# Kernel tuning notes

Hardware: AMD Instinct MI355X
Metric: run time of the kernel (lower is better)

Reference implementation:

```python
import jax, jax.numpy as jnp
import numpy as np

NUM_HEADS = 16
NUM_KV_GROUPS = 4
EPS = 1e-6


def _rms_norm(x, w):
    # normalize over last dim (head_dim)
    return x * jax.lax.rsqrt(jnp.mean(x * x, axis=-1, keepdims=True) + EPS) * w


def _rope_cos_sin(T, head_dim):
    half = head_dim // 2
    inv_freq = 1.0 / (10000.0 ** (jnp.arange(half, dtype=jnp.float32) / half))
    freqs = jnp.arange(T, dtype=jnp.float32)[:, None] * inv_freq[None, :]  # [T, half]
    cos = jnp.repeat(jnp.cos(freqs), 2, axis=-1)  # [T, head_dim]
    sin = jnp.repeat(jnp.sin(freqs), 2, axis=-1)
    return cos, sin


def _apply_rope(x, cos, sin):
    # x: [B, H, T, head_dim]; cos/sin broadcast over B,H
    x1 = x[..., ::2]
    x2 = x[..., 1::2]
    x_rot = jnp.stack([-x2, x1], axis=-1).reshape(x.shape)  # interleave (-x2, x1)
    return x * cos + x_rot * sin


def setup_inputs() -> dict:
    key = jax.random.key(0)
    ks = jax.random.split(key, 5)
    scale = lambda k, sh: jax.random.normal(k, sh, dtype=jnp.float32) * 0.02
    return {
        "x": jax.random.normal(ks[0], (4, 2048, 1024), dtype=jnp.float32),
        "Wq": scale(ks[1], (1024, 1024)),
        "Wk": scale(ks[2], (256, 1024)),
        "Wv": scale(ks[3], (256, 1024)),
        "Wo": scale(ks[4], (1024, 1024)),
        "qn_w": jnp.ones((64,), jnp.float32),
        "kn_w": jnp.ones((64,), jnp.float32),
    }


def reference(x, Wq, Wk, Wv, Wo, qn_w, kn_w):
    B, T, D = x.shape
    H, G = NUM_HEADS, NUM_KV_GROUPS
    hd = D // H

    # projections (torch Linear: y = x @ W.T), reshape to [B, heads, T, hd]
    q = (x @ Wq.T).reshape(B, T, H, hd).transpose(0, 2, 1, 3)
    k = (x @ Wk.T).reshape(B, T, G, hd).transpose(0, 2, 1, 3)
    v = (x @ Wv.T).reshape(B, T, G, hd).transpose(0, 2, 1, 3)

    # optional qk RMSNorm (qk_norm=True)
    q = _rms_norm(q, qn_w)
    k = _rms_norm(k, kn_w)

    # RoPE (position_offset = 0)
    cos, sin = _rope_cos_sin(T, hd)
    q = _apply_rope(q, cos, sin)
    k = _apply_rope(k, cos, sin)

    # GQA: expand kv heads to match query heads
    rep = H // G
    k = jnp.repeat(k, rep, axis=1)
    v = jnp.repeat(v, rep, axis=1)

    # causal SDPA
    scores = jnp.einsum('bhqd,bhkd->bhqk', q, k) / jnp.sqrt(jnp.float32(hd))
    causal = jnp.tril(jnp.ones((T, T), dtype=bool))
    scores = jnp.where(causal, scores, jnp.float32(-1e30))
    attn = jax.nn.softmax(scores, axis=-1)
    out = jnp.einsum('bhqk,bhkd->bhqd', attn, v)

    out = out.transpose(0, 2, 1, 3).reshape(B, T, D)
    return out @ Wo.T
```

## Files before the change

### kernel.cpp

```cpp
#include <hip/hip_runtime.h>

typedef unsigned short u16;
typedef __attribute__((ext_vector_type(8))) short bf16x8;
typedef __attribute__((ext_vector_type(4))) short bf16x4;
typedef __attribute__((ext_vector_type(4))) float f32x4;

#define GP(p) ((const __attribute__((address_space(1))) void*)(unsigned long long)(p))
#define LP(p) ((__attribute__((address_space(3))) void*)(unsigned int)(unsigned long long)(p))

#define QSCALE 0.180336879486998f
#define M_BIAS (-12.0f)

__device__ __forceinline__ u16 f2bf(float f) {
  union { float f; unsigned u; } v; v.f = f;
  unsigned r = v.u + 0x7fffu + ((v.u >> 16) & 1u);
  return (u16)(r >> 16);
}
__device__ __forceinline__ short f2bf_cvt(float f) {
  __bf16 b = (__bf16)f;
  return *reinterpret_cast<short*>(&b);
}

#if __has_builtin(__builtin_amdgcn_mfma_f32_16x16x16bf16_1k)
#define MFMA16(A, B, C) __builtin_amdgcn_mfma_f32_16x16x16bf16_1k((A), (B), (C), 0, 0, 0)
#elif __has_builtin(__builtin_amdgcn_mfma_f32_16x16x16_bf16)
#define MFMA16(A, B, C) __builtin_amdgcn_mfma_f32_16x16x16_bf16((A), (B), (C), 0, 0, 0)
#else
static __device__ __forceinline__ f32x4 mfma16_asm(bf16x4 a, bf16x4 b, f32x4 c) {
  asm volatile("v_mfma_f32_16x16x16_bf16 %0, %1, %2, %0" : "+v"(c) : "v"(a), "v"(b));
  return c;
}
#define MFMA16(A, B, C) mfma16_asm((A), (B), (C))
#endif

__global__ void cast_kernel(const float* __restrict__ in, u16* __restrict__ out, int n4) {
  int i = blockIdx.x * blockDim.x + threadIdx.x;
  int stride = gridDim.x * blockDim.x;
  for (; i < n4; i += stride) {
    float4 v = reinterpret_cast<const float4*>(in)[i];
    ushort4 o = make_ushort4(f2bf(v.x), f2bf(v.y), f2bf(v.z), f2bf(v.w));
    reinterpret_cast<ushort4*>(out)[i] = o;
  }
}

__global__ void cast_w_kernel(const float* __restrict__ Wq, const float* __restrict__ Wk,
                              const float* __restrict__ Wv, const float* __restrict__ Wo,
                              u16* __restrict__ Wcat, u16* __restrict__ Wob) {
  int i = blockIdx.x * 256 + threadIdx.x;
  const float* src; u16* dst; int off;
  if (i < 262144)      { src = Wq; dst = Wcat;           off = i; }
  else if (i < 327680) { src = Wk; dst = Wcat + 1048576; off = i - 262144; }
  else if (i < 393216) { src = Wv; dst = Wcat + 1310720; off = i - 327680; }
  else                 { src = Wo; dst = Wob;            off = i - 393216; }
  float4 v = reinterpret_cast<const float4*>(src)[off];
  reinterpret_cast<ushort4*>(dst)[off] =
      make_ushort4(f2bf(v.x), f2bf(v.y), f2bf(v.z), f2bf(v.w));
}

__global__ void rope_table_kernel(float* __restrict__ ctab, float* __restrict__ stab) {
  int i = blockIdx.x * 256 + threadIdx.x;
  int t = i >> 5, f = i & 31;
  float inv = exp2f((float)f * (-13.287712379549449f / 32.0f));
  float ang = (float)t * inv;
  float sv, cv;
  sincosf(ang, &sv, &cv);
  ctab[i] = cv;
  stab[i] = sv;
}

__launch_bounds__(256)
__global__ void gemm_qkv_kernel(const u16* __restrict__ A, const u16* __restrict__ W,
                                u16* __restrict__ qh, u16* __restrict__ kh,
                                u16* __restrict__ vh,
                                const float* __restrict__ qn_w, const float* __restrict__ kn_w,
                                const float* __restrict__ ctab, const float* __restrict__ stab) {
  __shared__ __align__(16) u16 As[128 * 64];
  __shared__ __align__(16) u16 Bs[128 * 64];
  const int tid = threadIdx.x;
  const int w = tid >> 6, l = tid & 63;
  const int lr = l & 15, lk = l >> 4;
  const int wr = w >> 1, wc = w & 1;
  const int m0 = blockIdx.x * 128, n0 = blockIdx.y * 128;
  f32x4 acc[4][4] = {};
  for (int k0 = 0; k0 < 1024; k0 += 64) {
#pragma unroll
    for (int i = 0; i < 4; ++i) {
      int c = i * 256 + tid;
      const u16* ga = A + (size_t)(m0 + (c >> 3)) * 1024 + k0 + (c & 7) * 8;
      __builtin_amdgcn_global_load_lds(GP(ga), LP((char*)As + (i * 256 + (tid & ~63)) * 16), 16, 0, 0);
      const u16* gb = W + (size_t)(n0 + (c >> 3)) * 1024 + k0 + (c & 7) * 8;
      __builtin_amdgcn_global_load_lds(GP(gb), LP((char*)Bs + (i * 256 + (tid & ~63)) * 16), 16, 0, 0);
    }
    asm volatile("s_waitcnt vmcnt(0)" ::: "memory");
    __syncthreads();
#pragma unroll
    for (int kk = 0; kk < 2; ++kk) {
      bf16x8 af[4], bfr[4];
#pragma unroll
      for (int fi = 0; fi < 4; ++fi)
        af[fi] = *reinterpret_cast<const bf16x8*>(&As[(wr * 64 + fi * 16 + lr) * 64 + kk * 32 + lk * 8]);
#pragma unroll
      for (int fj = 0; fj < 4; ++fj)
        bfr[fj] = *reinterpret_cast<const bf16x8*>(&Bs[(wc * 64 + fj * 16 + lr) * 64 + kk * 32 + lk * 8]);
#pragma unroll
      for (int fi = 0; fi < 4; ++fi)
#pragma unroll
        for (int fj = 0; fj < 4; ++fj)
          acc[fi][fj] = __builtin_amdgcn_mfma_f32_16x16x32_bf16(af[fi], bfr[fj], acc[fi][fj], 0, 0, 0);
    }
    __syncthreads();
  }
  const int ncol0 = n0 + wc * 64;
  if (ncol0 < 1280) {
    const bool isq = ncol0 < 1024;
    const float* wn = isq ? qn_w : kn_w;
    const float sc = isq ? QSCALE : 1.0f;
    float wv[4];
#pragma unroll
    for (int fj = 0; fj < 4; ++fj) wv[fj] = wn[fj * 16 + lr];
#pragma unroll
    for (int fi = 0; fi < 4; ++fi)
#pragma unroll
      for (int r = 0; r < 4; ++r) {
        float ss = 0.f;
#pragma unroll
        for (int fj = 0; fj < 4; ++fj) ss += acc[fi][fj][r] * acc[fi][fj][r];
        ss += __shfl_xor(ss, 1); ss += __shfl_xor(ss, 2);
        ss += __shfl_xor(ss, 4); ss += __shfl_xor(ss, 8);
        float rinv = rsqrtf(ss * (1.0f / 64.0f) + 1e-6f);
        int m = m0 + wr * 64 + fi * 16 + lk * 4 + r;
        int t = m & 2047, b = m >> 11;
#pragma unroll
        for (int fj = 0; fj < 4; ++fj) {
          float xn = acc[fi][fj][r] * rinv * wv[fj];
          float pr = __shfl_xor(xn, 1);
          float rot = (lr & 1) ? pr : -pr;
          int ci = t * 32 + fj * 8 + (lr >> 1);
          u16 outv = f2bf((xn * ctab[ci] + rot * stab[ci]) * sc);
          int n = ncol0 + fj * 16 + lr;
          if (isq) {
            int h = n >> 6, d = n & 63;
            qh[((size_t)((b * 16 + h) * 2048 + t)) * 64 + d] = outv;
          } else {
            int n2 = n - 1024, g = n2 >> 6, d = n2 & 63;
            kh[((size_t)((b * 4 + g) * 2048 + t)) * 64 + d] = outv;
          }
        }
      }
  } else {
#pragma unroll
    for (int fi = 0; fi < 4; ++fi)
#pragma unroll
      for (int fj = 0; fj < 4; ++fj)
#pragma unroll
        for (int r = 0; r < 4; ++r) {
          int m = m0 + wr * 64 + fi * 16 + lk * 4 + r;
          int n2 = ncol0 + fj * 16 + lr - 1280;
          int b = m >> 11, t = m & 2047;
          int g = n2 >> 6, d = n2 & 63;
          vh[((size_t)((b * 4 + g) * 2048 + t)) * 64 + d] = f2bf(acc[fi][fj][r]);
        }
  }
}

__launch_bounds__(256)
__global__ void vtrans_kernel(const u16* __restrict__ vh, u16* __restrict__ vt) {
  const int bg = blockIdx.y, t0 = blockIdx.x * 64;
  const u16* src = vh + ((size_t)bg * 2048 + t0) * 64;
  u16* dst = vt + (size_t)bg * 64 * 2048 + t0;
#pragma unroll
  for (int i = 0; i < 2; ++i) {
    int c = i * 256 + threadIdx.x;
    int d = c >> 3, kc = (c & 7) * 8;
    bf16x8 o;
#pragma unroll
    for (int j = 0; j < 8; ++j) o[j] = (short)src[(size_t)(kc + j) * 64 + d];
    *reinterpret_cast<bf16x8*>(&dst[(size_t)d * 2048 + kc]) = o;
  }
}

__launch_bounds__(256)
__global__ void attn_kernel(const u16* __restrict__ qh, const u16* __restrict__ kh,
                            const u16* __restrict__ vt, u16* __restrict__ ao) {
  __shared__ __align__(16) u16 Ks[2][64 * 64];
  __shared__ __align__(16) u16 Vts[2][64 * 64];
  const int tid = threadIdx.x, w = tid >> 6, l = tid & 63;
  const int lr = l & 15, lk = l >> 4;
  const int p = blockIdx.x, bh = blockIdx.y;
  const int b = bh >> 4, h = bh & 15, g = h >> 2;
  const u16* Qh = qh + ((size_t)((b * 16 + h) * 2048)) * 64;
  const u16* Kb = kh + ((size_t)((b * 4 + g) * 2048)) * 64;
  const u16* Vtb = vt + ((size_t)((b * 4 + g) * 64)) * 2048;
  const int swz = (lr & 7) * 8;

  auto stage = [&](int k0, int buf) {
#pragma unroll
    for (int i = 0; i < 2; ++i) {
      int c = i * 256 + tid;
      int row = c >> 3, scol = ((c & 7) ^ (row & 7)) * 8;
      const u16* gk = Kb + (size_t)(k0 + row) * 64 + scol;
      __builtin_amdgcn_global_load_lds(GP(gk), LP((char*)&Ks[buf][0] + (i * 256 + (tid & ~63)) * 16), 16, 0, 0);
      const u16* gv = Vtb + (size_t)row * 2048 + k0 + scol;
      __builtin_amdgcn_global_load_lds(GP(gv), LP((char*)&Vts[buf][0] + (i * 256 + (tid & ~63)) * 16), 16, 0, 0);
    }
  };

  int cur = 0;
  auto run_qtile = [&](int qt) {
    const int q0 = qt * 64;
    const u16* Qb = Qh + ((size_t)(q0 + w * 16)) * 64;
    const bf16x8 qf0 = *reinterpret_cast<const bf16x8*>(&Qb[lr * 64 + lk * 8]);
    const bf16x8 qf1 = *reinterpret_cast<const bf16x8*>(&Qb[lr * 64 + 32 + lk * 8]);
    f32x4 oacc[4] = {};
    float lrow = 0.f;
    stage(0, cur);
    asm volatile("s_waitcnt vmcnt(0)" ::: "memory");
    __builtin_amdgcn_s_barrier();
    for (int it = 0; it <= qt; ++it) {
      if (it < qt) stage((it + 1) * 64, cur ^ 1);
      f32x4 sacc[4];
#pragma unroll
      for (int fi = 0; fi < 4; ++fi)
#pragma unroll
        for (int r = 0; r < 4; ++r) sacc[fi][r] = M_BIAS;
      __builtin_amdgcn_s_setprio(1);
#pragma unroll
      for (int kk = 0; kk < 2; ++kk) {
        bf16x8 qf = kk ? qf1 : qf0;
#pragma unroll
        for (int fi = 0; fi < 4; ++fi) {
          bf16x8 kf = *reinterpret_cast<const bf16x8*>(
              &Ks[cur][(fi * 16 + lr) * 64 + ((kk * 32 + lk * 8) ^ swz)]);
          sacc[fi] = __builtin_amdgcn_mfma_f32_16x16x32_bf16(kf, qf, sacc[fi], 0, 0, 0);
        }
      }
      __builtin_amdgcn_s_setprio(0);
      if (it == qt) {
        int qloc = w * 16 + lr;
#pragma unroll
        for (int fi = 0; fi < 4; ++fi)
#pragma unroll
          for (int r = 0; r < 4; ++r)
            if (fi * 16 + lk * 4 + r > qloc) sacc[fi][r] = -1e30f;
      }
      float psum = 0.f;
      bf16x4 pb[4];
#pragma unroll
      for (int fi = 0; fi < 4; ++fi)
#pragma unroll
        for (int r = 0; r < 4; ++r) {
          float pv = exp2f(sacc[fi][r]);
          psum += pv;
          pb[fi][r] = f2bf_cvt(pv);
        }
      psum += __shfl_xor(psum, 16);
      psum += __shfl_xor(psum, 32);
      lrow += psum;
      __builtin_amdgcn_s_setprio(1);
#pragma unroll
      for (int fi = 0; fi < 4; ++fi)
#pragma unroll
        for (int db = 0; db < 4; ++db) {
          bf16x4 vf = *reinterpret_cast<const bf16x4*>(
              &Vts[cur][(db * 16 + lr) * 64 + ((fi * 16 + lk * 4) ^ swz)]);
          oacc[db] = MFMA16(vf, pb[fi], oacc[db]);
        }
      __builtin_amdgcn_s_setprio(0);
      asm volatile("s_waitcnt vmcnt(0)" ::: "memory");
      __builtin_amdgcn_s_barrier();
      cur ^= 1;
    }
    float inv = 1.0f / lrow;
#pragma unroll
    for (int db = 0; db < 4; ++db) {
      bf16x4 o;
#pragma unroll
      for (int r = 0; r < 4; ++r) o[r] = f2bf_cvt(oacc[db][r] * inv);
      *reinterpret_cast<bf16x4*>(
          &ao[((size_t)(b * 2048 + q0 + w * 16 + lr)) * 1024 + h * 64 + db * 16 + lk * 4]) = o;
    }
  };
  run_qtile(31 - p);
  run_qtile(p);
}

__launch_bounds__(256)
__global__ void gemm_out_kernel(const u16* __restrict__ A, const u16* __restrict__ W,
                                float* __restrict__ out) {
  __shared__ __align__(16) u16 As[128 * 64];
  __shared__ __align__(16) u16 Bs[128 * 64];
  const int tid = threadIdx.x;
  const int w = tid >> 6, l = tid & 63;
  const int lr = l & 15, lk = l >> 4;
  const int wr = w >> 1, wc = w & 1;
  const int m0 = blockIdx.x * 128, n0 = blockIdx.y * 128;
  f32x4 acc[4][4] = {};
  for (int k0 = 0; k0 < 1024; k0 += 64) {
#pragma unroll
    for (int i = 0; i < 4; ++i) {
      int c = i * 256 + tid;
      const u16* ga = A + (size_t)(m0 + (c >> 3)) * 1024 + k0 + (c & 7) * 8;
      __builtin_amdgcn_global_load_lds(GP(ga), LP((char*)As + (i * 256 + (tid & ~63)) * 16), 16, 0, 0);
      const u16* gb = W + (size_t)(n0 + (c >> 3)) * 1024 + k0 + (c & 7) * 8;
      __builtin_amdgcn_global_load_lds(GP(gb), LP((char*)Bs + (i * 256 + (tid & ~63)) * 16), 16, 0, 0);
    }
    asm volatile("s_waitcnt vmcnt(0)" ::: "memory");
    __syncthreads();
#pragma unroll
    for (int kk = 0; kk < 2; ++kk) {
      bf16x8 af[4], bfr[4];
#pragma unroll
      for (int fi = 0; fi < 4; ++fi)
        af[fi] = *reinterpret_cast<const bf16x8*>(&As[(wr * 64 + fi * 16 + lr) * 64 + kk * 32 + lk * 8]);
#pragma unroll
      for (int fj = 0; fj < 4; ++fj)
        bfr[fj] = *reinterpret_cast<const bf16x8*>(&Bs[(wc * 64 + fj * 16 + lr) * 64 + kk * 32 + lk * 8]);
#pragma unroll
      for (int fi = 0; fi < 4; ++fi)
#pragma unroll
        for (int fj = 0; fj < 4; ++fj)
          acc[fi][fj] = __builtin_amdgcn_mfma_f32_16x16x32_bf16(af[fi], bfr[fj], acc[fi][fj], 0, 0, 0);
    }
    __syncthreads();
  }
#pragma unroll
  for (int fi = 0; fi < 4; ++fi)
#pragma unroll
    for (int fj = 0; fj < 4; ++fj)
#pragma unroll
      for (int r = 0; r < 4; ++r) {
        int m = m0 + wr * 64 + fi * 16 + lk * 4 + r;
        int n = n0 + wc * 64 + fj * 16 + lr;
        out[(size_t)m * 1024 + n] = acc[fi][fj][r];
      }
}

extern "C" void kernel_launch(void* const* d_in, const int* in_sizes, int n_in,
                              void* d_out, int out_size, void* d_ws, size_t ws_size,
                              hipStream_t stream) {
  const float* x  = (const float*)d_in[0];
  const float* Wq = (const float*)d_in[1];
  const float* Wk = (const float*)d_in[2];
  const float* Wv = (const float*)d_in[3];
  const float* Wo = (const float*)d_in[4];
  const float* qn = (const float*)d_in[5];
  const float* kn = (const float*)d_in[6];
  float* out = (float*)d_out;
  char* ws = (char*)d_ws;
  u16* xb   = (u16*)(ws);
  u16* Wcat = (u16*)(ws + 16777216);
  u16* Wob  = (u16*)(ws + 19922944);
  u16* qh   = (u16*)(ws + 22020096);
  u16* kh   = (u16*)(ws + 38797312);
  u16* vh   = (u16*)(ws + 42991616);
  u16* ao   = (u16*)(ws + 47185920);
  u16* vtb  = xb;
  float* ctab = (float*)ao;
  float* stab = ctab + 65536;

  cast_kernel<<<2048, 256, 0, stream>>>(x, xb, 8388608 / 4);
  cast_w_kernel<<<2560, 256, 0, stream>>>(Wq, Wk, Wv, Wo, Wcat, Wob);
  rope_table_kernel<<<256, 256, 0, stream>>>(ctab, stab);
  dim3 g1(64, 12);
  gemm_qkv_kernel<<<g1, 256, 0, stream>>>(xb, Wcat, qh, kh, vh, qn, kn, ctab, stab);
  dim3 gv(32, 16);
  vtrans_kernel<<<gv, 256, 0, stream>>>(vh, vtb);
  dim3 ga(16, 64);
  attn_kernel<<<ga, 256, 0, stream>>>(qh, kh, vtb, ao);
  dim3 g2(64, 8);
  gemm_out_kernel<<<g2, 256, 0, stream>>>(ao, Wob, out);
}
```

Before: 184.7 us.

## Process paired causal query tiles together sharing each staged K/V tile

The attention kernel previously handled its two query tiles (31-p and p) one after the other, staging K/V tiles from global memory twice for the overlapping prefix. It now runs both tiles in a single pass over K/V: for the first qtB+1 key tiles each staged K/V block feeds MFMAs for both query tiles, and then only the longer tile continues. This removes roughly a third of the K/V global-to-LDS traffic and barriers and gives more independent MFMA work per LDS read. Staging pointers are also precomputed and advanced incrementally. The cost is higher register pressure from the two sets of accumulators, which could lower occupancy or cause spills.

```diff
diff --git a/kernel.cpp b/kernel.cpp
--- a/kernel.cpp
+++ b/kernel.cpp
@@ -10,6 +10,9 @@
 
 #define QSCALE 0.180336879486998f
 #define M_BIAS (-12.0f)
+
+struct TrueT  { static constexpr bool value = true;  };
+struct FalseT { static constexpr bool value = false; };
 
 __device__ __forceinline__ u16 f2bf(float f) {
   union { float f; unsigned u; } v; v.f = f;
@@ -188,89 +191,130 @@
   const int lr = l & 15, lk = l >> 4;
   const int p = blockIdx.x, bh = blockIdx.y;
   const int b = bh >> 4, h = bh & 15, g = h >> 2;
+  const int qtA = 31 - p, qtB = p;
   const u16* Qh = qh + ((size_t)((b * 16 + h) * 2048)) * 64;
   const u16* Kb = kh + ((size_t)((b * 4 + g) * 2048)) * 64;
   const u16* Vtb = vt + ((size_t)((b * 4 + g) * 64)) * 2048;
   const int swz = (lr & 7) * 8;
 
-  auto stage = [&](int k0, int buf) {
-#pragma unroll
-    for (int i = 0; i < 2; ++i) {
-      int c = i * 256 + tid;
-      int row = c >> 3, scol = ((c & 7) ^ (row & 7)) * 8;
-      const u16* gk = Kb + (size_t)(k0 + row) * 64 + scol;
-      __builtin_amdgcn_global_load_lds(GP(gk), LP((char*)&Ks[buf][0] + (i * 256 + (tid & ~63)) * 16), 16, 0, 0);
-      const u16* gv = Vtb + (size_t)row * 2048 + k0 + scol;
-      __builtin_amdgcn_global_load_lds(GP(gv), LP((char*)&Vts[buf][0] + (i * 256 + (tid & ~63)) * 16), 16, 0, 0);
-    }
+  const int c1 = 256 + tid;
+  const int r0 = tid >> 3, s0 = ((tid & 7) ^ (r0 & 7)) * 8;
+  const int r1 = c1 >> 3, s1 = ((c1 & 7) ^ (r1 & 7)) * 8;
+  const u16* kp0 = Kb + r0 * 64 + s0;
+  const u16* kp1 = Kb + r1 * 64 + s1;
+  const u16* vp0 = Vtb + (size_t)r0 * 2048 + s0;
+  const u16* vp1 = Vtb + (size_t)r1 * 2048 + s1;
+  char* kd = (char*)&Ks[0][0] + (tid & ~63) * 16;
+  char* vd = (char*)&Vts[0][0] + (tid & ~63) * 16;
+
+  auto stage = [&](int buf) {
+    __builtin_amdgcn_global_load_lds(GP(kp0), LP(kd + buf * 8192), 16, 0, 0);
+    __builtin_amdgcn_global_load_lds(GP(kp1), LP(kd + buf * 8192 + 4096), 16, 0, 0);
+    __builtin_amdgcn_global_load_lds(GP(vp0), LP(vd + buf * 8192), 16, 0, 0);
+    __builtin_amdgcn_global_load_lds(GP(vp1), LP(vd + buf * 8192 + 4096), 16, 0, 0);
+    kp0 += 64 * 64; kp1 += 64 * 64; vp0 += 64; vp1 += 64;
   };
 
+  const u16* QbA = Qh + (size_t)(qtA * 64 + w * 16) * 64;
+  const u16* QbB = Qh + (size_t)(qtB * 64 + w * 16) * 64;
+  const bf16x8 qfA0 = *reinterpret_cast<const bf16x8*>(&QbA[lr * 64 + lk * 8]);
+  const bf16x8 qfA1 = *reinterpret_cast<const bf16x8*>(&QbA[lr * 64 + 32 + lk * 8]);
+  const bf16x8 qfB0 = *reinterpret_cast<const bf16x8*>(&QbB[lr * 64 + lk * 8]);
+  const bf16x8 qfB1 = *reinterpret_cast<const bf16x8*>(&QbB[lr * 64 + 32 + lk * 8]);
+  f32x4 oaccA[4] = {}, oaccB[4] = {};
+  float lA = 0.f, lB = 0.f;
   int cur = 0;
-  auto run_qtile = [&](int qt) {
-    const int q0 = qt * 64;
-    const u16* Qb = Qh + ((size_t)(q0 + w * 16)) * 64;
-    const bf16x8 qf0 = *reinterpret_cast<const bf16x8*>(&Qb[lr * 64 + lk * 8]);
-    const bf16x8 qf1 = *reinterpret_cast<const bf16x8*>(&Qb[lr * 64 + 32 + lk * 8]);
-    f32x4 oacc[4] = {};
-    float lrow = 0.f;
-    stage(0, cur);
+
+  stage(0);
+  asm volatile("s_waitcnt vmcnt(0)" ::: "memory");
+  __builtin_amdgcn_s_barrier();
+
+  auto round = [&](int it, auto dual_tag) {
+    constexpr bool DUAL = decltype(dual_tag)::value;
+    if (it < qtA) stage(cur ^ 1);
+    f32x4 sA[4], sB[4];
+#pragma unroll
+    for (int fi = 0; fi < 4; ++fi)
+#pragma unroll
+      for (int r = 0; r < 4; ++r) {
+        sA[fi][r] = M_BIAS;
+        if constexpr (DUAL) sB[fi][r] = M_BIAS;
+      }
+    __builtin_amdgcn_s_setprio(1);
+#pragma unroll
+    for (int kk = 0; kk < 2; ++kk) {
+#pragma unroll
+      for (int fi = 0; fi < 4; ++fi) {
+        bf16x8 kf = *reinterpret_cast<const bf16x8*>(
+            &Ks[cur][(fi * 16 + lr) * 64 + ((kk * 32 + lk * 8) ^ swz)]);
+        sA[fi] = __builtin_amdgcn_mfma_f32_16x16x32_bf16(kf, kk ? qfA1 : qfA0, sA[fi], 0, 0, 0);
+        if constexpr (DUAL)
+          sB[fi] = __builtin_amdgcn_mfma_f32_16x16x32_bf16(kf, kk ? qfB1 : qfB0, sB[fi], 0, 0, 0);
+      }
+    }
+    __builtin_amdgcn_s_setprio(0);
+    const int qloc = w * 16 + lr;
+    if (it == qtA) {
+#pragma unroll
+      for (int fi = 0; fi < 4; ++fi)
+#pragma unroll
+        for (int r = 0; r < 4; ++r)
+          if (fi * 16 + lk * 4 + r > qloc) sA[fi][r] = -1e30f;
+    }
+    if constexpr (DUAL) {
+      if (it == qtB) {
+#pragma unroll
+        for (int fi = 0; fi < 4; ++fi)
+#pragma unroll
+          for (int r = 0; r < 4; ++r)
+            if (fi * 16 + lk * 4 + r > qloc) sB[fi][r] = -1e30f;
+      }
+    }
+    float psA = 0.f;
+    bf16x4 pbA[4], pbB[4];
+#pragma unroll
+    for (int fi = 0; fi < 4; ++fi)
+#pragma unroll
+      for (int r = 0; r < 4; ++r) {
+        float pv = exp2f(sA[fi][r]);
+        psA += pv;
+        pbA[fi][r] = f2bf_cvt(pv);
+      }
+    psA += __shfl_xor(psA, 16);
+    psA += __shfl_xor(psA, 32);
+    lA += psA;
+    if constexpr (DUAL) {
+      float psB = 0.f;
+#pragma unroll
+      for (int fi = 0; fi < 4; ++fi)
+#pragma unroll
+        for (int r = 0; r < 4; ++r) {
+          float pv = exp2f(sB[fi][r]);
+          psB += pv;
+          pbB[fi][r] = f2bf_cvt(pv);
+        }
+      psB += __shfl_xor(psB, 16);
+      psB += __shfl_xor(psB, 32);
+      lB += psB;
+    }
+    __builtin_amdgcn_s_setprio(1);
+#pragma unroll
+    for (int fi = 0; fi < 4; ++fi)
+#pragma unroll
+      for (int db = 0; db < 4; ++db) {
+        bf16x4 vf = *reinterpret_cast<const bf16x4*>(
+            &Vts[cur][(db * 16 + lr) * 64 + ((fi * 16 + lk * 4) ^ swz)]);
+        oaccA[db] = MFMA16(vf, pbA[fi], oaccA[db]);
+        if constexpr (DUAL) oaccB[db] = MFMA16(vf, pbB[fi], oaccB[db]);
+      }
+    __builtin_amdgcn_s_setprio(0);
     asm volatile("s_waitcnt vmcnt(0)" ::: "memory");
     __builtin_amdgcn_s_barrier();
-    for (int it = 0; it <= qt; ++it) {
-      if (it < qt) stage((it + 1) * 64, cur ^ 1);
-      f32x4 sacc[4];
-#pragma unroll
-      for (int fi = 0; fi < 4; ++fi)
-#pragma unroll
-        for (int r = 0; r < 4; ++r) sacc[fi][r] = M_BIAS;
-      __builtin_amdgcn_s_setprio(1);
-#pragma unroll
-      for (int kk = 0; kk < 2; ++kk) {
-        bf16x8 qf = kk ? qf1 : qf0;
-#pragma unroll
-        for (int fi = 0; fi < 4; ++fi) {
-          bf16x8 kf = *reinterpret_cast<const bf16x8*>(
-              &Ks[cur][(fi * 16 + lr) * 64 + ((kk * 32 + lk * 8) ^ swz)]);
-          sacc[fi] = __builtin_amdgcn_mfma_f32_16x16x32_bf16(kf, qf, sacc[fi], 0, 0, 0);
-        }
-      }
-      __builtin_amdgcn_s_setprio(0);
-      if (it == qt) {
-        int qloc = w * 16 + lr;
-#pragma unroll
-        for (int fi = 0; fi < 4; ++fi)
-#pragma unroll
-          for (int r = 0; r < 4; ++r)
-            if (fi * 16 + lk * 4 + r > qloc) sacc[fi][r] = -1e30f;
-      }
-      float psum = 0.f;
-      bf16x4 pb[4];
-#pragma unroll
-      for (int fi = 0; fi < 4; ++fi)
-#pragma unroll
-        for (int r = 0; r < 4; ++r) {
-          float pv = exp2f(sacc[fi][r]);
-          psum += pv;
-          pb[fi][r] = f2bf_cvt(pv);
-        }
-      psum += __shfl_xor(psum, 16);
-      psum += __shfl_xor(psum, 32);
-      lrow += psum;
-      __builtin_amdgcn_s_setprio(1);
-#pragma unroll
-      for (int fi = 0; fi < 4; ++fi)
-#pragma unroll
-        for (int db = 0; db < 4; ++db) {
-          bf16x4 vf = *reinterpret_cast<const bf16x4*>(
-              &Vts[cur][(db * 16 + lr) * 64 + ((fi * 16 + lk * 4) ^ swz)]);
-          oacc[db] = MFMA16(vf, pb[fi], oacc[db]);
-        }
-      __builtin_amdgcn_s_setprio(0);
-      asm volatile("s_waitcnt vmcnt(0)" ::: "memory");
-      __builtin_amdgcn_s_barrier();
-      cur ^= 1;
-    }
-    float inv = 1.0f / lrow;
+    cur ^= 1;
+  };
+
+  auto write_out = [&](const f32x4* oacc, float lsum, int q0) {
+    float inv = 1.0f / lsum;
 #pragma unroll
     for (int db = 0; db < 4; ++db) {
       bf16x4 o;
@@ -280,8 +324,11 @@
           &ao[((size_t)(b * 2048 + q0 + w * 16 + lr)) * 1024 + h * 64 + db * 16 + lk * 4]) = o;
     }
   };
-  run_qtile(31 - p);
-  run_qtile(p);
+
+  for (int it = 0; it <= qtB; ++it) round(it, TrueT{});
+  write_out(oaccB, lB, qtB * 64);
+  for (int it = qtB + 1; it <= qtA; ++it) round(it, FalseT{});
+  write_out(oaccA, lA, qtA * 64);
 }
 
 __launch_bounds__(256)
```

Measured after the change: 194.9 us. +5.5%, slower.
